# Optimization experiments

Hardware: AMD Instinct MI355X
Metric: run time of the kernel (lower is better)

The kernel has to match this reference:

```python
import jax, jax.numpy as jnp
import numpy as np

NEG_INF = -1e30


def setup_inputs() -> dict:
    key = jax.random.key(0)
    k1, k2 = jax.random.split(key)
    x = jax.random.normal(k1, (8, 512, 64, 64), dtype=jnp.float32)
    mask = jax.random.randint(k2, (64, 64), 0, 2, dtype=jnp.int32)  # 1 = masked (hole)
    return {"x": x, "mask": mask}


def reference(x, mask):
    # Shift-Net style random multi-shift (shift_sz=1, stride=1, triple_weight=1).
    # x: [B, C, H, W]; former = decoder half, latter = encoder half.
    B, C, H, W = x.shape
    c2 = C // 2
    HW = H * W
    former = x[:, :c2]
    latter = x[:, c2:]

    flag = mask.reshape(HW) > 0  # True where masked (needs filling)

    # Random neighbor selection: for every spatial position, pick a uniformly
    # random NON-masked source position (argmax of uniform scores with masked
    # sources disabled). Deterministic via fixed key, jit-friendly static shapes.
    rkey = jax.random.key(42)
    scores = jax.random.uniform(rkey, (HW, HW), dtype=jnp.float32)
    scores = jnp.where(flag[None, :], NEG_INF, scores)  # sources must be known region
    nb = jnp.argmax(scores, axis=1)  # [HW] random known-region index per position

    latter_flat = latter.reshape(B, c2, HW)
    gathered = latter_flat[:, :, nb]  # [B, c2, HW] shift-gathered encoder features
    # Paste gathered features only inside the masked region; zeros elsewhere.
    shift = jnp.where(flag[None, None, :], gathered, jnp.zeros_like(gathered))
    shift = shift.reshape(B, c2, H, W)

    return jnp.concatenate([former, latter, shift], axis=1)  # [B, 3C/2, H, W]
```

## Files before the change

### kernel.cpp

```cpp
#include <hip/hip_runtime.h>
#include <stdint.h>

static constexpr int HW = 4096;
static constexpr int CC = 512;
static constexpr int C2 = 256;
static constexpr int OC = 768;

__device__ __forceinline__ uint32_t rotl32(uint32_t x, int d) {
  return (x << d) | (x >> (32 - d));
}

__device__ __forceinline__ void threefry_0_42(uint32_t x0, uint32_t x1,
                                              uint32_t& o0, uint32_t& o1) {
  const uint32_t k0 = 0u;
  const uint32_t k1 = 42u;
  const uint32_t k2 = 0x1BD11BDAu ^ k0 ^ k1;
  x0 += k0; x1 += k1;
#define TF_ROUND(r) { x0 += x1; x1 = rotl32(x1, (r)); x1 ^= x0; }
  TF_ROUND(13) TF_ROUND(15) TF_ROUND(26) TF_ROUND(6)
  x0 += k1; x1 += k2 + 1u;
  TF_ROUND(17) TF_ROUND(29) TF_ROUND(16) TF_ROUND(24)
  x0 += k2; x1 += k0 + 2u;
  TF_ROUND(13) TF_ROUND(15) TF_ROUND(26) TF_ROUND(6)
  x0 += k0; x1 += k1 + 3u;
  TF_ROUND(17) TF_ROUND(29) TF_ROUND(16) TF_ROUND(24)
  x0 += k1; x1 += k2 + 4u;
  TF_ROUND(13) TF_ROUND(15) TF_ROUND(26) TF_ROUND(6)
  x0 += k2; x1 += k0 + 5u;
#undef TF_ROUND
  o0 = x0; o1 = x1;
}

__device__ __forceinline__ uint32_t jax_bits32(uint32_t e) {
  uint32_t o0, o1;
  threefry_0_42(0u, e, o0, o1);
  return o0 ^ o1;
}

__global__ __launch_bounds__(256) void nb_kernel(const int* __restrict__ mask,
                                                 int* __restrict__ idx) {
  const int i = blockIdx.x;
  const uint32_t e0 = (uint32_t)i * 4096u;
  long long best = -1;
#pragma unroll
  for (int q = 0; q < 16; ++q) {
    const int j = threadIdx.x + q * 256;
    const bool fl = mask[j] > 0;
    const uint32_t bits = jax_bits32(e0 + (uint32_t)j);
    if (!fl) {
      const long long k = ((long long)(bits >> 9) << 12) | (long long)(4095 - j);
      best = (k > best) ? k : best;
    }
  }
#pragma unroll
  for (int off = 32; off > 0; off >>= 1) {
    long long a = __shfl_down(best, off);
    best = (a > best) ? a : best;
  }
  __shared__ long long s[4];
  if ((threadIdx.x & 63) == 0) s[threadIdx.x >> 6] = best;
  __syncthreads();
  if (threadIdx.x == 0) {
    long long a = s[0];
#pragma unroll
    for (int w = 1; w < 4; ++w) if (s[w] > a) a = s[w];
    const int nb = (a >= 0) ? (4095 - (int)(a & 0xFFFLL)) : 0;
    idx[i] = (mask[i] > 0) ? nb : -1;
  }
}

__global__ __launch_bounds__(256) void out_kernel(const float* __restrict__ x,
                                                  const int* __restrict__ idx,
                                                  float* __restrict__ out) {
  const int p = blockIdx.x;
  if (p < 2048) {
    const int b = p >> 8, c = p & 255;
    const float* row = x + ((size_t)b * CC + C2 + c) * HW;
    float* orow = out + ((size_t)b * OC + 512 + c) * HW;
    __shared__ float lds[HW];
    const float4* row4 = (const float4*)row;
    float4* lds4 = (float4*)lds;
#pragma unroll
    for (int r = 0; r < 4; ++r) {
      const int t = threadIdx.x + r * 256;
      lds4[t] = row4[t];
    }
    __syncthreads();
    const int4* idx4 = (const int4*)idx;
    float4* orow4 = (float4*)orow;
#pragma unroll
    for (int r = 0; r < 4; ++r) {
      const int t = threadIdx.x + r * 256;
      const int4 nb = idx4[t];
      float4 v;
      v.x = (nb.x >= 0) ? lds[nb.x] : 0.0f;
      v.y = (nb.y >= 0) ? lds[nb.y] : 0.0f;
      v.z = (nb.z >= 0) ? lds[nb.z] : 0.0f;
      v.w = (nb.w >= 0) ? lds[nb.w] : 0.0f;
      orow4[t] = v;
    }
  } else {
    const int q = p - 2048;
    const int b = q >> 9, ch = q & 511;
    const float4* src = (const float4*)(x + ((size_t)b * CC + ch) * HW);
    float4* dst = (float4*)(out + ((size_t)b * OC + ch) * HW);
#pragma unroll
    for (int r = 0; r < 4; ++r) {
      const int t = threadIdx.x + r * 256;
      dst[t] = src[t];
    }
  }
}

extern "C" void kernel_launch(void* const* d_in, const int* in_sizes, int n_in,
                              void* d_out, int out_size, void* d_ws, size_t ws_size,
                              hipStream_t stream) {
  const float* x  = (const float*)d_in[0];
  const int* mask = (const int*)d_in[1];
  float* out      = (float*)d_out;
  int* idx        = (int*)d_ws;

  nb_kernel<<<4096, 256, 0, stream>>>(mask, idx);
  out_kernel<<<2048 + 4096, 256, 0, stream>>>(x, idx, out);
}
```

Measured before the change: 185.2 us.

## Compact unmasked columns, skip masked rows, overlap former copy with index search

A single-block prep kernel compacts the indices of unmasked source positions so the random-neighbour search hashes only valid columns, and rows that are not masked skip the search entirely. The copy of the former half is merged into the search kernel so it runs alongside the RNG work. The latter-half copy is fused into the gather kernel, which already loads each row into LDS. This cuts threefry evaluations roughly fourfold. The cost is an extra tiny serial launch, and the atomic compaction produces columns in nondeterministic order, which is safe here because the argmax key includes the column index.

```diff
diff --git a/kernel.cpp b/kernel.cpp
--- a/kernel.cpp
+++ b/kernel.cpp
@@ -37,78 +37,105 @@
   return o0 ^ o1;
 }
 
-__global__ __launch_bounds__(256) void nb_kernel(const int* __restrict__ mask,
-                                                 int* __restrict__ idx) {
-  const int i = blockIdx.x;
-  const uint32_t e0 = (uint32_t)i * 4096u;
-  long long best = -1;
+__global__ __launch_bounds__(256) void prep_kernel(const int* __restrict__ mask,
+                                                   int* __restrict__ mcount,
+                                                   int* __restrict__ cols) {
+  __shared__ int cnt;
+  if (threadIdx.x == 0) cnt = 0;
+  __syncthreads();
 #pragma unroll
   for (int q = 0; q < 16; ++q) {
     const int j = threadIdx.x + q * 256;
-    const bool fl = mask[j] > 0;
-    const uint32_t bits = jax_bits32(e0 + (uint32_t)j);
-    if (!fl) {
+    if (mask[j] == 0) {
+      const int pos = atomicAdd(&cnt, 1);
+      cols[pos] = j;
+    }
+  }
+  __syncthreads();
+  if (threadIdx.x == 0) *mcount = cnt;
+}
+
+__global__ __launch_bounds__(256) void rowcopy_kernel(const float* __restrict__ x,
+                                                      const int* __restrict__ mask,
+                                                      const int* __restrict__ mcount,
+                                                      const int* __restrict__ cols,
+                                                      int* __restrict__ idx,
+                                                      float* __restrict__ out) {
+  const int p = blockIdx.x;
+  if (p < 4096) {
+    const int i = p;
+    if (mask[i] == 0) {
+      if (threadIdx.x == 0) idx[i] = -1;
+      return;
+    }
+    const int m = *mcount;
+    const uint32_t e0 = (uint32_t)i * 4096u;
+    long long best = -1;
+    for (int t = threadIdx.x; t < m; t += 256) {
+      const int j = cols[t];
+      const uint32_t bits = jax_bits32(e0 + (uint32_t)j);
       const long long k = ((long long)(bits >> 9) << 12) | (long long)(4095 - j);
       best = (k > best) ? k : best;
     }
-  }
 #pragma unroll
-  for (int off = 32; off > 0; off >>= 1) {
-    long long a = __shfl_down(best, off);
-    best = (a > best) ? a : best;
-  }
-  __shared__ long long s[4];
-  if ((threadIdx.x & 63) == 0) s[threadIdx.x >> 6] = best;
-  __syncthreads();
-  if (threadIdx.x == 0) {
-    long long a = s[0];
+    for (int off = 32; off > 0; off >>= 1) {
+      long long a = __shfl_down(best, off);
+      best = (a > best) ? a : best;
+    }
+    __shared__ long long s[4];
+    if ((threadIdx.x & 63) == 0) s[threadIdx.x >> 6] = best;
+    __syncthreads();
+    if (threadIdx.x == 0) {
+      long long a = s[0];
 #pragma unroll
-    for (int w = 1; w < 4; ++w) if (s[w] > a) a = s[w];
-    const int nb = (a >= 0) ? (4095 - (int)(a & 0xFFFLL)) : 0;
-    idx[i] = (mask[i] > 0) ? nb : -1;
-  }
-}
-
-__global__ __launch_bounds__(256) void out_kernel(const float* __restrict__ x,
-                                                  const int* __restrict__ idx,
-                                                  float* __restrict__ out) {
-  const int p = blockIdx.x;
-  if (p < 2048) {
-    const int b = p >> 8, c = p & 255;
-    const float* row = x + ((size_t)b * CC + C2 + c) * HW;
-    float* orow = out + ((size_t)b * OC + 512 + c) * HW;
-    __shared__ float lds[HW];
-    const float4* row4 = (const float4*)row;
-    float4* lds4 = (float4*)lds;
-#pragma unroll
-    for (int r = 0; r < 4; ++r) {
-      const int t = threadIdx.x + r * 256;
-      lds4[t] = row4[t];
-    }
-    __syncthreads();
-    const int4* idx4 = (const int4*)idx;
-    float4* orow4 = (float4*)orow;
-#pragma unroll
-    for (int r = 0; r < 4; ++r) {
-      const int t = threadIdx.x + r * 256;
-      const int4 nb = idx4[t];
-      float4 v;
-      v.x = (nb.x >= 0) ? lds[nb.x] : 0.0f;
-      v.y = (nb.y >= 0) ? lds[nb.y] : 0.0f;
-      v.z = (nb.z >= 0) ? lds[nb.z] : 0.0f;
-      v.w = (nb.w >= 0) ? lds[nb.w] : 0.0f;
-      orow4[t] = v;
+      for (int w = 1; w < 4; ++w) if (s[w] > a) a = s[w];
+      idx[i] = (a >= 0) ? (4095 - (int)(a & 0xFFFLL)) : 0;
     }
   } else {
-    const int q = p - 2048;
-    const int b = q >> 9, ch = q & 511;
-    const float4* src = (const float4*)(x + ((size_t)b * CC + ch) * HW);
-    float4* dst = (float4*)(out + ((size_t)b * OC + ch) * HW);
+    const int q = p - 4096;
+    const int b = q >> 8, c = q & 255;
+    const float4* src = (const float4*)(x + ((size_t)b * CC + c) * HW);
+    float4* dst = (float4*)(out + ((size_t)b * OC + c) * HW);
 #pragma unroll
     for (int r = 0; r < 4; ++r) {
       const int t = threadIdx.x + r * 256;
       dst[t] = src[t];
     }
+  }
+}
+
+__global__ __launch_bounds__(256) void latter_kernel(const float* __restrict__ x,
+                                                     const int* __restrict__ idx,
+                                                     float* __restrict__ out) {
+  const int p = blockIdx.x;
+  const int b = p >> 8, c = p & 255;
+  const float* row = x + ((size_t)b * CC + C2 + c) * HW;
+  float* ocopy  = out + ((size_t)b * OC + 256 + c) * HW;
+  float* oshift = out + ((size_t)b * OC + 512 + c) * HW;
+  __shared__ float lds[HW];
+  const float4* row4 = (const float4*)row;
+  float4* lds4 = (float4*)lds;
+  float4* ocopy4 = (float4*)ocopy;
+#pragma unroll
+  for (int r = 0; r < 4; ++r) {
+    const int t = threadIdx.x + r * 256;
+    const float4 v = row4[t];
+    lds4[t] = v;
+    ocopy4[t] = v;
+  }
+  __syncthreads();
+  const int4* idx4 = (const int4*)idx;
+  float4* oshift4 = (float4*)oshift;
+#pragma unroll
+  for (int r = 0; r < 4; ++r) {
+    const int t = threadIdx.x + r * 256;
+    const int4 nb = idx4[t];
+    float4 v;
+    v.x = (nb.x >= 0) ? lds[nb.x] : 0.0f;
+    v.y = (nb.y >= 0) ? lds[nb.y] : 0.0f;
+    v.z = (nb.z >= 0) ? lds[nb.z] : 0.0f;
+    v.w = (nb.w >= 0) ? lds[nb.w] : 0.0f;
+    oshift4[t] = v;
   }
 }
 
@@ -119,7 +146,10 @@
   const int* mask = (const int*)d_in[1];
   float* out      = (float*)d_out;
   int* idx        = (int*)d_ws;
+  int* mcount     = idx + 4096;
+  int* cols       = mcount + 1;
 
-  nb_kernel<<<4096, 256, 0, stream>>>(mask, idx);
-  out_kernel<<<2048 + 4096, 256, 0, stream>>>(x, idx, out);
+  prep_kernel<<<1, 256, 0, stream>>>(mask, mcount, cols);
+  rowcopy_kernel<<<4096 + 2048, 256, 0, stream>>>(x, mask, mcount, cols, idx, out);
+  latter_kernel<<<2048, 256, 0, stream>>>(x, idx, out);
 }
```

Result: faster. 169.8 us (-8.3%).

## Skip argmax for unmasked rows, compact known columns, overlap with passthrough copy

Applied to the files above, without the earlier changes.

The neighbor-index argmax is now computed only for masked positions, and only over a compacted list of unmasked source columns built with ballot and prefix scan, which roughly halves the threefry hashing work. That argmax work is interleaved with the passthrough copy blocks in a single launch, so the copy's memory traffic can overlap the compute-heavy RNG. The gather runs as a separate second kernel. The cost is extra shared memory and synchronisation for the compaction, plus a larger and more divergent first kernel.

```diff
diff --git a/kernel.cpp b/kernel.cpp
--- a/kernel.cpp
+++ b/kernel.cpp
@@ -37,70 +37,12 @@
   return o0 ^ o1;
 }
 
-__global__ __launch_bounds__(256) void nb_kernel(const int* __restrict__ mask,
-                                                 int* __restrict__ idx) {
-  const int i = blockIdx.x;
-  const uint32_t e0 = (uint32_t)i * 4096u;
-  long long best = -1;
-#pragma unroll
-  for (int q = 0; q < 16; ++q) {
-    const int j = threadIdx.x + q * 256;
-    const bool fl = mask[j] > 0;
-    const uint32_t bits = jax_bits32(e0 + (uint32_t)j);
-    if (!fl) {
-      const long long k = ((long long)(bits >> 9) << 12) | (long long)(4095 - j);
-      best = (k > best) ? k : best;
-    }
-  }
-#pragma unroll
-  for (int off = 32; off > 0; off >>= 1) {
-    long long a = __shfl_down(best, off);
-    best = (a > best) ? a : best;
-  }
-  __shared__ long long s[4];
-  if ((threadIdx.x & 63) == 0) s[threadIdx.x >> 6] = best;
-  __syncthreads();
-  if (threadIdx.x == 0) {
-    long long a = s[0];
-#pragma unroll
-    for (int w = 1; w < 4; ++w) if (s[w] > a) a = s[w];
-    const int nb = (a >= 0) ? (4095 - (int)(a & 0xFFFLL)) : 0;
-    idx[i] = (mask[i] > 0) ? nb : -1;
-  }
-}
-
-__global__ __launch_bounds__(256) void out_kernel(const float* __restrict__ x,
-                                                  const int* __restrict__ idx,
-                                                  float* __restrict__ out) {
+__global__ __launch_bounds__(256) void copy_argmax_kernel(
+    const float* __restrict__ x, const int* __restrict__ mask,
+    int* __restrict__ idx, float* __restrict__ out) {
   const int p = blockIdx.x;
-  if (p < 2048) {
-    const int b = p >> 8, c = p & 255;
-    const float* row = x + ((size_t)b * CC + C2 + c) * HW;
-    float* orow = out + ((size_t)b * OC + 512 + c) * HW;
-    __shared__ float lds[HW];
-    const float4* row4 = (const float4*)row;
-    float4* lds4 = (float4*)lds;
-#pragma unroll
-    for (int r = 0; r < 4; ++r) {
-      const int t = threadIdx.x + r * 256;
-      lds4[t] = row4[t];
-    }
-    __syncthreads();
-    const int4* idx4 = (const int4*)idx;
-    float4* orow4 = (float4*)orow;
-#pragma unroll
-    for (int r = 0; r < 4; ++r) {
-      const int t = threadIdx.x + r * 256;
-      const int4 nb = idx4[t];
-      float4 v;
-      v.x = (nb.x >= 0) ? lds[nb.x] : 0.0f;
-      v.y = (nb.y >= 0) ? lds[nb.y] : 0.0f;
-      v.z = (nb.z >= 0) ? lds[nb.z] : 0.0f;
-      v.w = (nb.w >= 0) ? lds[nb.w] : 0.0f;
-      orow4[t] = v;
-    }
-  } else {
-    const int q = p - 2048;
+  if ((p & 1) == 0) {
+    const int q = p >> 1;
     const int b = q >> 9, ch = q & 511;
     const float4* src = (const float4*)(x + ((size_t)b * CC + ch) * HW);
     float4* dst = (float4*)(out + ((size_t)b * OC + ch) * HW);
@@ -109,6 +51,105 @@
       const int t = threadIdx.x + r * 256;
       dst[t] = src[t];
     }
+    return;
+  }
+  const int i = p >> 1;
+  if (mask[i] == 0) {
+    if (threadIdx.x == 0) idx[i] = -1;
+    return;
+  }
+
+  __shared__ int cols[HW];
+  __shared__ int chunk_cnt[64];
+  __shared__ int chunk_off[64];
+  __shared__ int total_sh;
+  const int wave = threadIdx.x >> 6;
+  const int lane = threadIdx.x & 63;
+
+#pragma unroll
+  for (int t = wave; t < 64; t += 4) {
+    const int j = t * 64 + lane;
+    const unsigned long long bal = __ballot(mask[j] == 0);
+    if (lane == 0) chunk_cnt[t] = __popcll(bal);
+  }
+  __syncthreads();
+  if (wave == 0) {
+    int v = chunk_cnt[lane];
+    int inc = v;
+#pragma unroll
+    for (int off = 1; off < 64; off <<= 1) {
+      const int u = __shfl_up(inc, off);
+      if (lane >= off) inc += u;
+    }
+    chunk_off[lane] = inc - v;
+    if (lane == 63) total_sh = inc;
+  }
+  __syncthreads();
+#pragma unroll
+  for (int t = wave; t < 64; t += 4) {
+    const int j = t * 64 + lane;
+    const bool un = (mask[j] == 0);
+    const unsigned long long bal = __ballot(un);
+    if (un) {
+      const int pos = chunk_off[t] + __popcll(bal & ((1ULL << lane) - 1ULL));
+      cols[pos] = j;
+    }
+  }
+  __syncthreads();
+
+  const int m = total_sh;
+  const uint32_t e0 = (uint32_t)i * 4096u;
+  long long best = -1;
+  for (int t = threadIdx.x; t < m; t += 256) {
+    const int j = cols[t];
+    const uint32_t bits = jax_bits32(e0 + (uint32_t)j);
+    const long long k = ((long long)(bits >> 9) << 12) | (long long)(4095 - j);
+    best = (k > best) ? k : best;
+  }
+#pragma unroll
+  for (int off = 32; off > 0; off >>= 1) {
+    const long long a = __shfl_down(best, off);
+    best = (a > best) ? a : best;
+  }
+  __shared__ long long s[4];
+  if (lane == 0) s[wave] = best;
+  __syncthreads();
+  if (threadIdx.x == 0) {
+    long long a = s[0];
+#pragma unroll
+    for (int w = 1; w < 4; ++w) if (s[w] > a) a = s[w];
+    idx[i] = (a >= 0) ? (4095 - (int)(a & 0xFFFLL)) : 0;
+  }
+}
+
+__global__ __launch_bounds__(256) void gather_kernel(const float* __restrict__ x,
+                                                     const int* __restrict__ idx,
+                                                     float* __restrict__ out) {
+  const int p = blockIdx.x;
+  const int b = p >> 8, c = p & 255;
+  const float* row = x + ((size_t)b * CC + C2 + c) * HW;
+  float* oshift = out + ((size_t)b * OC + 512 + c) * HW;
+  __shared__ float lds[HW];
+  const float4* row4 = (const float4*)row;
+  float4* lds4 = (float4*)lds;
+#pragma unroll
+  for (int r = 0; r < 4; ++r) {
+    const int t = threadIdx.x + r * 256;
+    lds4[t] = row4[t];
+  }
+  __syncthreads();
+  const int4* idx4 = (const int4*)idx;
+  float4* oshift4 = (float4*)oshift;
+#pragma unroll
+  for (int r = 0; r < 4; ++r) {
+    const int t = threadIdx.x + r * 256;
+    const int4 nb = idx4[t];
+    float4 v;
+    v.x = (nb.x >= 0) ? lds[nb.x] : 0.0f;
+    v.y = (nb.y >= 0) ? lds[nb.y] : 0.0f;
+    v.z = (nb.z >= 0) ? lds[nb.z] : 0.0f;
+    v.w = (nb.w >= 0) ? lds[nb.w] : 0.0f;
+    oshift4[t] = v;
   }
 }
 
@@ -120,6 +161,6 @@
   float* out      = (float*)d_out;
   int* idx        = (int*)d_ws;
 
-  nb_kernel<<<4096, 256, 0, stream>>>(mask, idx);
-  out_kernel<<<2048 + 4096, 256, 0, stream>>>(x, idx, out);
+  copy_argmax_kernel<<<8192, 256, 0, stream>>>(x, mask, idx, out);
+  gather_kernel<<<2048, 256, 0, stream>>>(x, idx, out);
 }
```

Measured after the change: 163.0 us (median of 2 runs). 1.14x faster.
